# Optimization experiments

Hardware: AMD Instinct MI355X
Metric: run time of the kernel (lower is better)

The kernel has to match this reference:

```python
import jax, jax.numpy as jnp
import numpy as np

# Dims implied by init: input_dim=128, b_dim=64 -> per-branch Mamba d_model=16
D_MODEL = 16
D_STATE = 16
D_CONV = 4
D_INNER = 32   # expand * d_model
DT_RANK = 1    # ceil(d_model / 16)
EPS = 1e-5


def _ln(x, g, b):
    m = x.mean(-1, keepdims=True)
    v = x.var(-1, keepdims=True)
    return (x - m) / jnp.sqrt(v + EPS) * g + b


def _gn(x, g, b, groups):
    B, C, H, W = x.shape
    xr = x.reshape(B, groups, C // groups, H, W)
    m = xr.mean((2, 3, 4), keepdims=True)
    v = xr.var((2, 3, 4), keepdims=True)
    xr = (xr - m) / jnp.sqrt(v + EPS)
    return xr.reshape(B, C, H, W) * g[None, :, None, None] + b[None, :, None, None]


def _mamba(u, in_proj_w, conv_w, conv_b, x_proj_w, dt_proj_w, dt_proj_b, A_log, Dp, out_proj_w):
    # u: [N, L, d_model]
    N, L, _ = u.shape
    xz = u @ in_proj_w.T                       # [N, L, 2*d_inner]
    xc, zg = jnp.split(xz, 2, axis=-1)
    # causal depthwise conv1d over L
    xt = xc.transpose(0, 2, 1)                 # [N, d_inner, L]
    xt = jax.lax.conv_general_dilated(
        xt, conv_w, (1,), [(D_CONV - 1, 0)],
        dimension_numbers=('NCH', 'OIH', 'NCH'),
        feature_group_count=D_INNER)
    xt = xt + conv_b[None, :, None]
    xc = jax.nn.silu(xt).transpose(0, 2, 1)    # [N, L, d_inner]
    x_dbl = xc @ x_proj_w.T                    # [N, L, dt_rank + 2*d_state]
    dt = x_dbl[..., :DT_RANK]
    Bv = x_dbl[..., DT_RANK:DT_RANK + D_STATE]
    Cv = x_dbl[..., DT_RANK + D_STATE:]
    dt = jax.nn.softplus(dt @ dt_proj_w.T + dt_proj_b)  # [N, L, d_inner]
    A = -jnp.exp(A_log)                        # [d_inner, d_state]

    def step(h, inp):
        dt_t, B_t, C_t, x_t = inp              # [N,di],[N,ds],[N,ds],[N,di]
        dA = jnp.exp(dt_t[:, :, None] * A)     # [N, di, ds]
        h = dA * h + (dt_t * x_t)[:, :, None] * B_t[:, None, :]
        y = jnp.einsum('nds,ns->nd', h, C_t)
        return h, y

    h0 = jnp.zeros((N, D_INNER, D_STATE), u.dtype)
    xs = (dt.transpose(1, 0, 2), Bv.transpose(1, 0, 2),
          Cv.transpose(1, 0, 2), xc.transpose(1, 0, 2))
    _, ys = jax.lax.scan(step, h0, xs)         # ys: [L, N, d_inner]
    y = ys.transpose(1, 0, 2) + xc * Dp        # skip via D
    y = y * jax.nn.silu(zg)
    return y @ out_proj_w.T                    # [N, L, d_model]


def _forward(x, pre_ln_g, pre_ln_b, bott_in_w, bott_in_b,
             in_proj_w, conv_w, conv_b, x_proj_w, dt_proj_w, dt_proj_b,
             A_log, Dp, out_proj_w, post_ln_g, post_ln_b,
             bott_out_w, bott_out_b, res_scale,
             fc1_w, gn1_g, gn1_b, fc2_w, gn2_g, gn2_b):
    B, C, H, W = x.shape
    L = H * W
    # ---- PVMLayer token mixer ----
    xf = x.reshape(B, C, L).transpose(0, 2, 1)            # [B, L, C]
    z = _ln(xf, pre_ln_g, pre_ln_b)
    z = z @ bott_in_w.T + bott_in_b                       # [B, L, 64]
    # four chunks share the same Mamba weights -> batch them together
    zc = z.reshape(B, L, 4, D_MODEL).transpose(2, 0, 1, 3).reshape(4 * B, L, D_MODEL)
    m = _mamba(zc, in_proj_w, conv_w, conv_b, x_proj_w, dt_proj_w, dt_proj_b,
               A_log, Dp, out_proj_w) + zc
    z = m.reshape(4, B, L, D_MODEL).transpose(1, 2, 0, 3).reshape(B, L, 4 * D_MODEL)
    z = _ln(z, post_ln_g, post_ln_b)
    z = (z @ bott_out_w.T + bott_out_b) * res_scale       # [B, L, C]
    token = z.transpose(0, 2, 1).reshape(B, C, H, W)
    mixed = x + token                                     # PVMLayer residual (eval: drop_path=id)
    out = x + mixed                                       # PVMFormer residual
    # ---- Mlp (1x1 conv + GroupNorm) ----
    h = jnp.einsum('bchw,oc->bohw', out, fc1_w)
    h = _gn(h, gn1_g, gn1_b, 32)
    h = jax.nn.gelu(h, approximate=False)
    h = jnp.einsum('bchw,oc->bohw', h, fc2_w)
    h = _gn(h, gn2_g, gn2_b, 32)
    return out + h


def setup_inputs() -> dict:
    key = jax.random.key(0)
    ks = jax.random.split(key, 16)
    n = lambda k, s, sc=0.02: jax.random.normal(k, s, jnp.float32) * sc
    C = 128
    return {
        'x': jax.random.normal(ks[0], (8, C, 64, 64), jnp.float32),
        'pre_ln_g': jnp.ones((C,), jnp.float32),
        'pre_ln_b': jnp.zeros((C,), jnp.float32),
        'bott_in_w': n(ks[1], (64, C)),
        'bott_in_b': jnp.zeros((64,), jnp.float32),
        'in_proj_w': n(ks[2], (2 * D_INNER, D_MODEL)),
        'conv_w': n(ks[3], (D_INNER, 1, D_CONV), 0.1),
        'conv_b': jnp.zeros((D_INNER,), jnp.float32),
        'x_proj_w': n(ks[4], (DT_RANK + 2 * D_STATE, D_INNER)),
        'dt_proj_w': n(ks[5], (D_INNER, DT_RANK), 0.5),
        'dt_proj_b': n(ks[6], (D_INNER,), 0.5),
        'A_log': jnp.log(jnp.broadcast_to(jnp.arange(1.0, D_STATE + 1.0, dtype=jnp.float32), (D_INNER, D_STATE))),
        'Dp': jnp.ones((D_INNER,), jnp.float32),
        'out_proj_w': n(ks[7], (D_MODEL, D_INNER)),
        'post_ln_g': jnp.ones((64,), jnp.float32),
        'post_ln_b': jnp.zeros((64,), jnp.float32),
        'bott_out_w': n(ks[8], (C, 64)),
        'bott_out_b': jnp.zeros((C,), jnp.float32),
        'res_scale': jnp.array(0.5, jnp.float32),
        'fc1_w': n(ks[9], (4 * C, C)),
        'gn1_g': jnp.ones((4 * C,), jnp.float32),
        'gn1_b': jnp.zeros((4 * C,), jnp.float32),
        'fc2_w': n(ks[10], (C, 4 * C)),
        'gn2_g': jnp.ones((C,), jnp.float32),
        'gn2_b': jnp.zeros((C,), jnp.float32),
    }


def reference(x, pre_ln_g, pre_ln_b, bott_in_w, bott_in_b,
              in_proj_w, conv_w, conv_b, x_proj_w, dt_proj_w, dt_proj_b,
              A_log, Dp, out_proj_w, post_ln_g, post_ln_b,
              bott_out_w, bott_out_b, res_scale,
              fc1_w, gn1_g, gn1_b, fc2_w, gn2_g, gn2_b):
    return _forward(x, pre_ln_g, pre_ln_b, bott_in_w, bott_in_b,
                    in_proj_w, conv_w, conv_b, x_proj_w, dt_proj_w, dt_proj_b,
                    A_log, Dp, out_proj_w, post_ln_g, post_ln_b,
                    bott_out_w, bott_out_b, res_scale,
                    fc1_w, gn1_g, gn1_b, fc2_w, gn2_g, gn2_b)
```

## Files before the change

kernel.cpp:

```cpp
#include <hip/hip_runtime.h>
#include <hip/hip_bf16.h>
#include <math.h>

#define L4K 4096
#define NCH 32
#define CL  128
#define SPN (128*4096)

typedef __attribute__((ext_vector_type(8))) short short8;
typedef __attribute__((ext_vector_type(4))) float f32x4;

__device__ __forceinline__ unsigned short f2b(float f) {
    unsigned int u = __float_as_uint(f);
    unsigned int r = u + 0x7FFFu + ((u >> 16) & 1u);
    return (unsigned short)(r >> 16);
}
__device__ __forceinline__ float b2f(unsigned short h) {
    return __uint_as_float(((unsigned int)h) << 16);
}
__device__ __forceinline__ float rowsum16(float p) {
    int t;
    t = __builtin_amdgcn_update_dpp(0, __float_as_int(p), 0x128, 0xf, 0xf, true);
    p += __int_as_float(t);
    t = __builtin_amdgcn_update_dpp(0, __float_as_int(p), 0x124, 0xf, 0xf, true);
    p += __int_as_float(t);
    t = __builtin_amdgcn_update_dpp(0, __float_as_int(p), 0x122, 0xf, 0xf, true);
    p += __int_as_float(t);
    t = __builtin_amdgcn_update_dpp(0, __float_as_int(p), 0x121, 0xf, 0xf, true);
    p += __int_as_float(t);
    return p;
}

__global__ __launch_bounds__(256) void k1_pre(
    const float* __restrict__ x, const float* __restrict__ png, const float* __restrict__ pnb,
    const float* __restrict__ biw, const float* __restrict__ bib, const float* __restrict__ ipw,
    float* __restrict__ zc, float* __restrict__ xcp, float* __restrict__ zg)
{
    __shared__ float xs[128*32];
    __shared__ float wl[64*128];
    __shared__ float zs[32*65];
    __shared__ float ipl[64*16];
    __shared__ float pngs[128], pnbs[128];
    int tid = threadIdx.x;
    int l0 = blockIdx.x*32, b = blockIdx.y;
    const float* xb = x + (size_t)b*128*L4K;
    for (int it = 0; it < 16; ++it) {
        int f = it*256 + tid; int c = f>>5, i = f&31;
        xs[f] = xb[(size_t)c*L4K + l0 + i];
    }
    for (int f = tid; f < 8192; f += 256) wl[f] = biw[f];
    for (int f = tid; f < 1024; f += 256) ipl[f] = ipw[f];
    if (tid < 128) { pngs[tid] = png[tid]; pnbs[tid] = pnb[tid]; }
    __syncthreads();
    int i = tid & 31, q = tid >> 5;
    float s = 0.f, s2 = 0.f;
    for (int c = 0; c < 128; ++c) { float v = xs[c*32+i]; s += v; s2 = fmaf(v,v,s2); }
    float mn = s*(1.f/128.f);
    float rstd = rsqrtf(s2*(1.f/128.f) - mn*mn + 1e-5f);
    float z[8];
    #pragma unroll
    for (int jj = 0; jj < 8; ++jj) z[jj] = bib[q*8+jj];
    for (int c = 0; c < 128; ++c) {
        float xv = (xs[c*32+i] - mn)*rstd*pngs[c] + pnbs[c];
        #pragma unroll
        for (int jj = 0; jj < 8; ++jj) z[jj] = fmaf(xv, wl[(q*8+jj)*128 + c], z[jj]);
    }
    #pragma unroll
    for (int jj = 0; jj < 8; ++jj) zs[i*65 + q*8 + jj] = z[jj];
    __syncthreads();
    if (tid < 128) {
        int i2 = tid & 31, g = tid >> 5;
        int n = g*8 + b; int l = l0 + i2;
        float zv[16];
        #pragma unroll
        for (int k = 0; k < 16; ++k) zv[k] = zs[i2*65 + g*16 + k];
        float* zcb = zc + ((size_t)n*16)*L4K + l;
        #pragma unroll
        for (int k = 0; k < 16; ++k) zcb[(size_t)k*L4K] = zv[k];
        float* xo = xcp + ((size_t)n*32)*L4K + l;
        float* zo = zg  + ((size_t)n*32)*L4K + l;
        #pragma unroll
        for (int o = 0; o < 64; ++o) {
            float a = 0.f;
            #pragma unroll
            for (int k = 0; k < 16; ++k) a = fmaf(zv[k], ipl[o*16+k], a);
            if (o < 32) xo[(size_t)o*L4K] = a; else zo[(size_t)(o-32)*L4K] = a;
        }
    }
}

__global__ __launch_bounds__(128) void k2_conv(
    const float* __restrict__ xcp, const float* __restrict__ cw, const float* __restrict__ cb,
    const float* __restrict__ xpw, const float* __restrict__ dtw, const float* __restrict__ dtb,
    float* __restrict__ S)
{
    __shared__ float xt[131*33];
    __shared__ float cwl[128], cbl[32], xpl[33*32], dtwl[32], dtbl[32];
    int tid = threadIdx.x;
    int t0 = blockIdx.x*128; int n = blockIdx.y;
    const float* xb = xcp + (size_t)n*32*L4K;
    #pragma unroll 4
    for (int d = 0; d < 32; ++d) {
        int t = t0 - 3 + tid;
        xt[tid*33 + d] = (t >= 0) ? xb[(size_t)d*L4K + t] : 0.f;
        if (tid < 3) {
            int r = 128 + tid; int t2 = t0 - 3 + r;
            xt[r*33 + d] = xb[(size_t)d*L4K + t2];
        }
    }
    if (tid < 128) cwl[tid] = cw[tid];
    if (tid < 32) { cbl[tid] = cb[tid]; dtwl[tid] = dtw[tid]; dtbl[tid] = dtb[tid]; }
    for (int f = tid; f < 33*32; f += 128) xpl[f] = xpw[f];
    __syncthreads();
    int t = t0 + tid;
    float xc[32];
    #pragma unroll
    for (int d = 0; d < 32; ++d) {
        float sv = cbl[d];
        #pragma unroll
        for (int k = 0; k < 4; ++k) sv = fmaf(cwl[d*4+k], xt[(tid+k)*33 + d], sv);
        xc[d] = sv / (1.f + __expf(-sv));
    }
    float dtr = 0.f; float Bv[16], Cv[16];
    #pragma unroll
    for (int dd = 0; dd < 32; ++dd) dtr = fmaf(xc[dd], xpl[dd], dtr);
    #pragma unroll
    for (int o = 0; o < 16; ++o) {
        float a = 0.f, a2 = 0.f;
        #pragma unroll
        for (int dd = 0; dd < 32; ++dd) {
            a  = fmaf(xc[dd], xpl[(1+o)*32+dd],  a);
            a2 = fmaf(xc[dd], xpl[(17+o)*32+dd], a2);
        }
        Bv[o] = a; Cv[o] = a2;
    }
    float* Sn = S + (size_t)n*SPN + t;
    #pragma unroll
    for (int d = 0; d < 32; ++d) {
        float dv = fmaf(dtr, dtwl[d], dtbl[d]);
        float sp = fmaxf(dv, 0.f) + log1pf(__expf(-fabsf(dv)));
        Sn[(size_t)d*L4K]      = sp;
        Sn[(size_t)(32+d)*L4K] = sp * xc[d];
        Sn[(size_t)(96+d)*L4K] = xc[d];
    }
    #pragma unroll
    for (int o = 0; o < 16; ++o) {
        Sn[(size_t)(64+o)*L4K] = Bv[o];
        Sn[(size_t)(80+o)*L4K] = Cv[o];
    }
}

__global__ __launch_bounds__(512) void k3a_local(
    const float* __restrict__ S, const float* __restrict__ alog,
    float* __restrict__ chunkA, float* __restrict__ chunkH)
{
    __shared__ float2 pDT[32*130];
    __shared__ float  pB[16*132];
    int tid = threadIdx.x;
    int d = tid >> 4, s = tid & 15;
    int chunk = blockIdx.x, n = blockIdx.y;
    float A = -__expf(alog[d*16 + s]);
    const float* base = S + (size_t)n*SPN + (size_t)chunk*CL;
    {
        int sd = tid >> 4, j = tid & 15;
        const float* dtp = base + (size_t)sd*L4K + j*8;
        const float* dxp = base + (size_t)(32+sd)*L4K + j*8;
        float4 a0 = *(const float4*)(dtp);
        float4 a1 = *(const float4*)(dtp+4);
        float4 b0 = *(const float4*)(dxp);
        float4 b1 = *(const float4*)(dxp+4);
        float2* w = pDT + sd*130 + j*8;
        *(float4*)(w+0) = make_float4(a0.x,b0.x,a0.y,b0.y);
        *(float4*)(w+2) = make_float4(a0.z,b0.z,a0.w,b0.w);
        *(float4*)(w+4) = make_float4(a1.x,b1.x,a1.y,b1.y);
        *(float4*)(w+6) = make_float4(a1.z,b1.z,a1.w,b1.w);
    }
    if (tid < 256) {
        int ss = tid >> 4, j = tid & 15;
        const float* bp = base + (size_t)(64+ss)*L4K + j*8;
        float4 v0 = *(const float4*)(bp);
        float4 v1 = *(const float4*)(bp+4);
        float* w = pB + ss*132 + j*8;
        *(float4*)(w+0) = v0;
        *(float4*)(w+4) = v1;
    }
    __syncthreads();
    float h = 0.f, ap = 1.f;
    #pragma unroll 4
    for (int t = 0; t < CL; ++t) {
        float2 dd = pDT[d*130 + t];
        float Bv = pB[s*132 + t];
        float dA = __expf(dd.x * A);
        h = fmaf(dA, h, dd.y * Bv);
        ap *= dA;
    }
    size_t idx = (size_t)chunk*16384 + n*512 + tid;
    chunkA[idx] = ap;
    chunkH[idx] = h;
}

__global__ __launch_bounds__(256) void k3b_prefix(
    const float* __restrict__ chunkA, const float* __restrict__ chunkH,
    float* __restrict__ hstart)
{
    int nds = blockIdx.x*256 + threadIdx.x;
    float h = 0.f;
    hstart[nds] = 0.f;
    for (int c = 0; c < NCH-1; ++c) {
        h = fmaf(h, chunkA[(size_t)c*16384 + nds], chunkH[(size_t)c*16384 + nds]);
        hstart[(size_t)(c+1)*16384 + nds] = h;
    }
}

__global__ __launch_bounds__(512) void k3c_emit(
    const float* __restrict__ S, const float* __restrict__ alog,
    const float* __restrict__ hstart, float* __restrict__ y)
{
    __shared__ float2 pDT[32*130];
    __shared__ float2 pBC[16*130];
    int tid = threadIdx.x;
    int d = tid >> 4, s = tid & 15;
    int chunk = blockIdx.x, n = blockIdx.y;
    float A = -__expf(alog[d*16 + s]);
    const float* base = S + (size_t)n*SPN + (size_t)chunk*CL;
    float h = hstart[(size_t)chunk*16384 + n*512 + tid];
    {
        int sd = tid >> 4, j = tid & 15;
        const float* dtp = base + (size_t)sd*L4K + j*8;
        const float* dxp = base + (size_t)(32+sd)*L4K + j*8;
        float4 a0 = *(const float4*)(dtp);
        float4 a1 = *(const float4*)(dtp+4);
        float4 b0 = *(const float4*)(dxp);
        float4 b1 = *(const float4*)(dxp+4);
        float2* w = pDT + sd*130 + j*8;
        *(float4*)(w+0) = make_float4(a0.x,b0.x,a0.y,b0.y);
        *(float4*)(w+2) = make_float4(a0.z,b0.z,a0.w,b0.w);
        *(float4*)(w+4) = make_float4(a1.x,b1.x,a1.y,b1.y);
        *(float4*)(w+6) = make_float4(a1.z,b1.z,a1.w,b1.w);
    }
    if (tid < 256) {
        int ss = tid >> 4, j = tid & 15;
        const float* bp = base + (size_t)(64+ss)*L4K + j*8;
        const float* cp = base + (size_t)(80+ss)*L4K + j*8;
        float4 v0 = *(const float4*)(bp);
        float4 v1 = *(const float4*)(bp+4);
        float4 c0 = *(const float4*)(cp);
        float4 c1 = *(const float4*)(cp+4);
        float2* w = pBC + ss*130 + j*8;
        *(float4*)(w+0) = make_float4(v0.x,c0.x,v0.y,c0.y);
        *(float4*)(w+2) = make_float4(v0.z,c0.z,v0.w,c0.w);
        *(float4*)(w+4) = make_float4(v1.x,c1.x,v1.y,c1.y);
        *(float4*)(w+6) = make_float4(v1.z,c1.z,v1.w,c1.w);
    }
    __syncthreads();
    float4* yb = (float4*)(y + ((size_t)n*32 + d)*L4K + (size_t)chunk*CL);
    for (int i = 0; i < CL/4; ++i) {
        float4 yv;
        #pragma unroll
        for (int u = 0; u < 4; ++u) {
            int t = i*4 + u;
            float2 dd = pDT[d*130 + t];
            float2 bc = pBC[s*130 + t];
            float dA = __expf(dd.x * A);
            h = fmaf(dA, h, dd.y * bc.x);
            ((float*)&yv)[u] = rowsum16(h * bc.y);
        }
        if (s == 0) yb[i] = yv;
    }
}

__global__ __launch_bounds__(256) void k5_out(
    const float* __restrict__ y, const float* __restrict__ S, const float* __restrict__ zg,
    const float* __restrict__ zc, const float* __restrict__ Dp, const float* __restrict__ opw,
    float* __restrict__ m)
{
    int id = blockIdx.x*256 + threadIdx.x;
    int n = id >> 12, t = id & 4095;
    const float* yb  = y  + (size_t)n*32*L4K + t;
    const float* xcb = S  + (size_t)n*SPN + (size_t)96*L4K + t;
    const float* zgb = zg + (size_t)n*32*L4K + t;
    const float* zcb = zc + (size_t)n*16*L4K + t;
    float v[32];
    #pragma unroll
    for (int dd = 0; dd < 32; ++dd) {
        float g = zgb[(size_t)dd*L4K];
        float sig = 1.f/(1.f + __expf(-g));
        v[dd] = (yb[(size_t)dd*L4K] + xcb[(size_t)dd*L4K]*Dp[dd]) * (g*sig);
    }
    int b = n & 7, g4 = n >> 3;
    float* mp = m + ((size_t)b*64 + g4*16)*L4K + t;
    #pragma unroll
    for (int j = 0; j < 16; ++j) {
        float a = zcb[(size_t)j*L4K];
        #pragma unroll
        for (int dd = 0; dd < 32; ++dd) a = fmaf(v[dd], opw[j*32+dd], a);
        mp[(size_t)j*L4K] = a;
    }
}

__global__ __launch_bounds__(256) void k6_post(
    const float* __restrict__ m, const float* __restrict__ x,
    const float* __restrict__ pog, const float* __restrict__ pob,
    const float* __restrict__ bow, const float* __restrict__ bob,
    const float* __restrict__ rsp, float* __restrict__ outp,
    unsigned short* __restrict__ outpb)
{
    __shared__ float ms[64*65];
    __shared__ float wl[128*64];
    __shared__ float pogs[64], pobs[64];
    int tid = threadIdx.x;
    int l0 = blockIdx.x*64, b = blockIdx.y;
    for (int f = tid; f < 4096; f += 256) {
        int i = f & 63, j = f >> 6;
        ms[i*65 + j] = m[((size_t)b*64 + j)*L4K + l0 + i];
    }
    for (int f = tid; f < 8192; f += 256) wl[f] = bow[f];
    if (tid < 64) { pogs[tid] = pog[tid]; pobs[tid] = pob[tid]; }
    __syncthreads();
    float rs = rsp[0];
    int i = tid & 63, q = tid >> 6;
    float s = 0.f, s2 = 0.f;
    for (int j = 0; j < 64; ++j) { float v = ms[i*65+j]; s += v; s2 = fmaf(v,v,s2); }
    float mn = s*(1.f/64.f);
    float rstd = rsqrtf(s2*(1.f/64.f) - mn*mn + 1e-5f);
    float acc[32];
    #pragma unroll
    for (int cc = 0; cc < 32; ++cc) acc[cc] = bob[q*32+cc];
    for (int j = 0; j < 64; ++j) {
        float v = (ms[i*65+j]-mn)*rstd*pogs[j] + pobs[j];
        #pragma unroll
        for (int cc = 0; cc < 32; ++cc) acc[cc] = fmaf(v, wl[(q*32+cc)*64+j], acc[cc]);
    }
    const float* xb = x + (size_t)b*128*L4K + l0 + i;
    float* ob = outp + (size_t)b*128*L4K + l0 + i;
    unsigned short pk[32];
    #pragma unroll
    for (int cc = 0; cc < 32; ++cc) {
        int c = q*32 + cc;
        float val = 2.f*xb[(size_t)c*L4K] + acc[cc]*rs;
        ob[(size_t)c*L4K] = val;
        pk[cc] = f2b(val);
    }
    uint4* op = (uint4*)&outpb[((size_t)b*L4K + l0 + i)*128 + q*32];
    #pragma unroll
    for (int u = 0; u < 4; ++u) {
        uint4 v;
        v.x = pk[u*8+0] | ((unsigned)pk[u*8+1]<<16);
        v.y = pk[u*8+2] | ((unsigned)pk[u*8+3]<<16);
        v.z = pk[u*8+4] | ((unsigned)pk[u*8+5]<<16);
        v.w = pk[u*8+6] | ((unsigned)pk[u*8+7]<<16);
        op[u] = v;
    }
}

template<int KCHUNKS, bool OUT_BF16>
__global__ __launch_bounds__(256) void gemm_mfma(
    const unsigned short* __restrict__ Ab, const float* __restrict__ Wg,
    void* __restrict__ Dout, int Kpitch, int Npitch)
{
    __shared__ char lds[65536];
    int tid = threadIdx.x;
    int lane = tid & 63, w = tid >> 6;
    int l0 = blockIdx.x * 128, n0 = blockIdx.y * 128, b = blockIdx.z;
    size_t arow0 = (size_t)b*L4K + l0;
    int wm = (w>>1)*64, wn = (w&1)*64;
    f32x4 acc[4][4] = {};
    char* aL = lds;
    char* wL = lds + 32768;
    for (int kc = 0; kc < KCHUNKS; ++kc) {
        if (kc) __syncthreads();
        #pragma unroll
        for (int it = 0; it < 8; ++it) {
            int f = it*256 + tid;
            int row = f >> 4, kp = f & 15;
            uint4 v = *(const uint4*)&Ab[(arow0 + row)*(size_t)Kpitch + kc*128 + kp*8];
            int off = row*256 + kp*16; off ^= (row&7)<<4;
            *(uint4*)(aL + off) = v;
        }
        #pragma unroll
        for (int it = 0; it < 16; ++it) {
            int f = it*256 + tid;
            int row = f >> 5, kg = f & 31;
            float4 v = *(const float4*)&Wg[(size_t)(n0+row)*(KCHUNKS*128) + kc*128 + kg*4];
            uint2 p;
            p.x = f2b(v.x) | ((unsigned)f2b(v.y)<<16);
            p.y = f2b(v.z) | ((unsigned)f2b(v.w)<<16);
            int off = row*256 + kg*8; off ^= (row&7)<<4;
            *(uint2*)(wL + off) = p;
        }
        __syncthreads();
        #pragma unroll
        for (int ks = 0; ks < 4; ++ks) {
            short8 af[4], wf[4];
            int kb = ks*64 + (lane>>4)*16;
            #pragma unroll
            for (int mi = 0; mi < 4; ++mi) {
                int row = wm + mi*16 + (lane&15);
                int off = row*256 + kb; off ^= (row&7)<<4;
                af[mi] = *(const short8*)(aL + off);
            }
            #pragma unroll
            for (int ni = 0; ni < 4; ++ni) {
                int row = wn + ni*16 + (lane&15);
                int off = row*256 + kb; off ^= (row&7)<<4;
                wf[ni] = *(const short8*)(wL + off);
            }
            #pragma unroll
            for (int mi = 0; mi < 4; ++mi)
                #pragma unroll
                for (int ni = 0; ni < 4; ++ni)
                    acc[mi][ni] = __builtin_amdgcn_mfma_f32_16x16x32_bf16(af[mi], wf[ni], acc[mi][ni], 0, 0, 0);
        }
    }
    if (OUT_BF16) {
        __syncthreads();
        unsigned short* cL = (unsigned short*)lds;
        #pragma unroll
        for (int mi = 0; mi < 4; ++mi)
            #pragma unroll
            for (int ni = 0; ni < 4; ++ni)
                #pragma unroll
                for (int r = 0; r < 4; ++r) {
                    int row = wm + mi*16 + (lane>>4)*4 + r;
                    int col = wn + ni*16 + (lane&15);
                    cL[row*136 + col] = f2b(acc[mi][ni][r]);
                }
        __syncthreads();
        unsigned short* D = (unsigned short*)Dout;
        #pragma unroll
        for (int it = 0; it < 8; ++it) {
            int f = it*256 + tid;
            int row = f >> 4, kp = f & 15;
            uint4 v = *(const uint4*)&cL[row*136 + kp*8];
            *(uint4*)&D[(arow0 + row)*(size_t)Npitch + n0 + kp*8] = v;
        }
    } else {
        float* D = (float*)Dout;
        #pragma unroll
        for (int mi = 0; mi < 4; ++mi)
            #pragma unroll
            for (int ni = 0; ni < 4; ++ni)
                #pragma unroll
                for (int r = 0; r < 4; ++r) {
                    int row = wm + mi*16 + (lane>>4)*4 + r;
                    int col = wn + ni*16 + (lane&15);
                    D[(arow0 + row)*(size_t)Npitch + n0 + col] = acc[mi][ni][r];
                }
    }
}

__global__ __launch_bounds__(256) void k_gn1stats(
    const unsigned short* __restrict__ h, float* __restrict__ stats)
{
    __shared__ float sred[256], sred2[256];
    int tid = threadIdx.x;
    int b = blockIdx.x >> 5, g = blockIdx.x & 31;
    float s = 0.f, s2 = 0.f;
    for (int it = 0; it < 32; ++it) {
        int f = it*256 + tid;
        int l = f >> 1, half = f & 1;
        uint4 v = *(const uint4*)&h[((size_t)b*L4K + l)*512 + g*16 + half*8];
        unsigned int ws[4] = {v.x, v.y, v.z, v.w};
        #pragma unroll
        for (int u = 0; u < 4; ++u) {
            float a = b2f((unsigned short)(ws[u] & 0xFFFF));
            float c = b2f((unsigned short)(ws[u] >> 16));
            s += a + c; s2 = fmaf(a,a,s2); s2 = fmaf(c,c,s2);
        }
    }
    sred[tid] = s; sred2[tid] = s2; __syncthreads();
    for (int off = 128; off; off >>= 1) {
        if (tid < off) { sred[tid] += sred[tid+off]; sred2[tid] += sred2[tid+off]; }
        __syncthreads();
    }
    if (tid == 0) {
        float inv = 1.f/65536.f;
        float mn = sred[0]*inv;
        float var = sred2[0]*inv - mn*mn;
        stats[blockIdx.x*2]   = mn;
        stats[blockIdx.x*2+1] = rsqrtf(var + 1e-5f);
    }
}

__global__ __launch_bounds__(256) void k9_gngelu(
    unsigned short* __restrict__ h, const float* __restrict__ stats,
    const float* __restrict__ g1, const float* __restrict__ b1)
{
    size_t idx = ((size_t)blockIdx.x*256 + threadIdx.x)*8;
    int o0 = (int)(idx & 511);
    int b = (int)(idx >> 21);
    int sg = b*32 + (o0 >> 4);
    float mn = stats[sg*2], rstd = stats[sg*2+1];
    uint4 v = *(uint4*)&h[idx];
    unsigned int ws[4] = {v.x, v.y, v.z, v.w};
    unsigned int out[4];
    #pragma unroll
    for (int u = 0; u < 4; ++u) {
        float a = b2f((unsigned short)(ws[u] & 0xFFFF));
        float c = b2f((unsigned short)(ws[u] >> 16));
        int o = o0 + u*2;
        float ta = (a-mn)*rstd*g1[o]   + b1[o];
        float tc = (c-mn)*rstd*g1[o+1] + b1[o+1];
        ta = 0.5f*ta*(1.f + erff(ta*0.70710678118654752f));
        tc = 0.5f*tc*(1.f + erff(tc*0.70710678118654752f));
        out[u] = f2b(ta) | ((unsigned)f2b(tc)<<16);
    }
    uint4 r; r.x = out[0]; r.y = out[1]; r.z = out[2]; r.w = out[3];
    *(uint4*)&h[idx] = r;
}

__global__ __launch_bounds__(256) void k_gn2stats(
    const float* __restrict__ h, float* __restrict__ stats)
{
    __shared__ float sred[256], sred2[256];
    int tid = threadIdx.x;
    int b = blockIdx.x >> 5, g = blockIdx.x & 31;
    float s = 0.f, s2 = 0.f;
    for (int it = 0; it < 16; ++it) {
        int l = it*256 + tid;
        float4 v = ((const float4*)h)[((size_t)b*L4K + l)*32 + g];
        s += v.x+v.y+v.z+v.w;
        s2 = fmaf(v.x,v.x,s2); s2 = fmaf(v.y,v.y,s2); s2 = fmaf(v.z,v.z,s2); s2 = fmaf(v.w,v.w,s2);
    }
    sred[tid] = s; sred2[tid] = s2; __syncthreads();
    for (int off = 128; off; off >>= 1) {
        if (tid < off) { sred[tid] += sred[tid+off]; sred2[tid] += sred2[tid+off]; }
        __syncthreads();
    }
    if (tid == 0) {
        float inv = 1.f/16384.f;
        float mn = sred[0]*inv;
        float var = sred2[0]*inv - mn*mn;
        stats[blockIdx.x*2]   = mn;
        stats[blockIdx.x*2+1] = rsqrtf(var + 1e-5f);
    }
}

__global__ __launch_bounds__(256) void k12_final(
    const float* __restrict__ outp, const float* __restrict__ h2t,
    const float* __restrict__ stats, const float* __restrict__ g2,
    const float* __restrict__ b2, float* __restrict__ out)
{
    __shared__ float T[32*33];
    int tid = threadIdx.x;
    int l0 = blockIdx.x*32, c0 = blockIdx.y*32, b = blockIdx.z;
    {
        int i = tid >> 3, jq = tid & 7;
        float4 v = ((const float4*)h2t)[((size_t)b*L4K + l0 + i)*32 + (c0>>2) + jq];
        int sg = b*32 + (c0>>2) + jq;
        float mn = stats[sg*2], rstd = stats[sg*2+1];
        int c = c0 + jq*4;
        T[(jq*4+0)*33 + i] = (v.x-mn)*rstd*g2[c+0] + b2[c+0];
        T[(jq*4+1)*33 + i] = (v.y-mn)*rstd*g2[c+1] + b2[c+1];
        T[(jq*4+2)*33 + i] = (v.z-mn)*rstd*g2[c+2] + b2[c+2];
        T[(jq*4+3)*33 + i] = (v.w-mn)*rstd*g2[c+3] + b2[c+3];
    }
    __syncthreads();
    {
        int c = tid >> 3, iq = tid & 7;
        size_t gi = ((size_t)b*128 + c0 + c)*1024 + (l0>>2) + iq;
        float4 o = ((const float4*)outp)[gi];
        float4 r;
        r.x = o.x + T[c*33 + iq*4 + 0];
        r.y = o.y + T[c*33 + iq*4 + 1];
        r.z = o.z + T[c*33 + iq*4 + 2];
        r.w = o.w + T[c*33 + iq*4 + 3];
        ((float4*)out)[gi] = r;
    }
}

extern "C" void kernel_launch(void* const* d_in, const int* in_sizes, int n_in,
                              void* d_out, int out_size, void* d_ws, size_t ws_size,
                              hipStream_t stream) {
    (void)in_sizes; (void)n_in; (void)out_size; (void)ws_size;
    const float* x    = (const float*)d_in[0];
    const float* png  = (const float*)d_in[1];
    const float* pnb  = (const float*)d_in[2];
    const float* biw  = (const float*)d_in[3];
    const float* bib  = (const float*)d_in[4];
    const float* ipw  = (const float*)d_in[5];
    const float* cw   = (const float*)d_in[6];
    const float* cb   = (const float*)d_in[7];
    const float* xpw  = (const float*)d_in[8];
    const float* dtw  = (const float*)d_in[9];
    const float* dtb  = (const float*)d_in[10];
    const float* alog = (const float*)d_in[11];
    const float* Dp   = (const float*)d_in[12];
    const float* opw  = (const float*)d_in[13];
    const float* pog  = (const float*)d_in[14];
    const float* pob  = (const float*)d_in[15];
    const float* bow  = (const float*)d_in[16];
    const float* bob  = (const float*)d_in[17];
    const float* rsp  = (const float*)d_in[18];
    const float* f1w  = (const float*)d_in[19];
    const float* g1g  = (const float*)d_in[20];
    const float* g1b  = (const float*)d_in[21];
    const float* f2w  = (const float*)d_in[22];
    const float* g2g  = (const float*)d_in[23];
    const float* g2b  = (const float*)d_in[24];

    char* ws = (char*)d_ws;
    float* S    = (float*)(ws + 0);
    float* zc   = (float*)(ws + 67108864);
    float* zg   = (float*)(ws + 75497472);
    float* xcp  = (float*)(ws + 92274688);
    float* y    = (float*)(ws + 92274688);
    float* m    = (float*)(ws + 109051904);
    float* chA  = (float*)(ws + 109051904);
    float* chH  = (float*)(ws + 109051904 + 2097152);
    float* hst  = (float*)(ws + 109051904 + 4194304);
    float*          outp  = (float*)(ws + 0);
    unsigned short* outpb = (unsigned short*)(ws + 16777216);
    unsigned short* h1tb  = (unsigned short*)(ws + 25165824);
    float*          h2t   = (float*)(ws + 58720256);
    float*          st1   = (float*)(ws + 75497472);
    float*          st2   = (float*)(ws + 75501568);

    k1_pre<<<dim3(128,8),256,0,stream>>>(x,png,pnb,biw,bib,ipw,zc,xcp,zg);
    k2_conv<<<dim3(32,32),128,0,stream>>>(xcp,cw,cb,xpw,dtw,dtb,S);
    k3a_local<<<dim3(NCH,32),512,0,stream>>>(S,alog,chA,chH);
    k3b_prefix<<<64,256,0,stream>>>(chA,chH,hst);
    k3c_emit<<<dim3(NCH,32),512,0,stream>>>(S,alog,hst,y);
    k5_out<<<512,256,0,stream>>>(y,S,zg,zc,Dp,opw,m);
    k6_post<<<dim3(64,8),256,0,stream>>>(m,x,pog,pob,bow,bob,rsp,outp,outpb);
    gemm_mfma<1,true><<<dim3(32,4,8),256,0,stream>>>(outpb,f1w,(void*)h1tb,128,512);
    k_gn1stats<<<256,256,0,stream>>>(h1tb,st1);
    k9_gngelu<<<8192,256,0,stream>>>(h1tb,st1,g1g,g1b);
    gemm_mfma<4,false><<<dim3(32,1,8),256,0,stream>>>(h1tb,f2w,(void*)h2t,512,128);
    k_gn2stats<<<256,256,0,stream>>>(h2t,st2);
    k12_final<<<dim3(128,4,8),256,0,stream>>>(outp,h2t,st2,g2g,g2b,(float*)d_out);
}
```

Baseline: 392.9 us.

## Trim registers in conv and output kernels, halve GEMM2 tile, approximate GELU

k2_conv drops its shared-memory weight staging, reads weights straight from global memory, and computes the B and C projections in two separate loops to lower register pressure. k5_out splits each timestep's work across two threads through shared memory and launches twice the blocks. The second GEMM uses 64-row tiles so it runs twice as many blocks. The erf-based GELU is replaced with the tanh approximation built on fast exp, which changes numerics slightly.

```diff
diff --git a/kernel.cpp b/kernel.cpp
--- a/kernel.cpp
+++ b/kernel.cpp
@@ -95,7 +95,6 @@
     float* __restrict__ S)
 {
     __shared__ float xt[131*33];
-    __shared__ float cwl[128], cbl[32], xpl[33*32], dtwl[32], dtbl[32];
     int tid = threadIdx.x;
     int t0 = blockIdx.x*128; int n = blockIdx.y;
     const float* xb = xcp + (size_t)n*32*L4K;
@@ -103,50 +102,44 @@
     for (int d = 0; d < 32; ++d) {
         int t = t0 - 3 + tid;
         xt[tid*33 + d] = (t >= 0) ? xb[(size_t)d*L4K + t] : 0.f;
-        if (tid < 3) {
-            int r = 128 + tid; int t2 = t0 - 3 + r;
-            xt[r*33 + d] = xb[(size_t)d*L4K + t2];
-        }
-    }
-    if (tid < 128) cwl[tid] = cw[tid];
-    if (tid < 32) { cbl[tid] = cb[tid]; dtwl[tid] = dtw[tid]; dtbl[tid] = dtb[tid]; }
-    for (int f = tid; f < 33*32; f += 128) xpl[f] = xpw[f];
-    __syncthreads();
-    int t = t0 + tid;
+        if (tid < 3) xt[(128+tid)*33 + d] = xb[(size_t)d*L4K + t0 + 125 + tid];
+    }
+    __syncthreads();
     float xc[32];
     #pragma unroll
     for (int d = 0; d < 32; ++d) {
-        float sv = cbl[d];
-        #pragma unroll
-        for (int k = 0; k < 4; ++k) sv = fmaf(cwl[d*4+k], xt[(tid+k)*33 + d], sv);
-        xc[d] = sv / (1.f + __expf(-sv));
-    }
-    float dtr = 0.f; float Bv[16], Cv[16];
-    #pragma unroll
-    for (int dd = 0; dd < 32; ++dd) dtr = fmaf(xc[dd], xpl[dd], dtr);
-    #pragma unroll
-    for (int o = 0; o < 16; ++o) {
-        float a = 0.f, a2 = 0.f;
-        #pragma unroll
-        for (int dd = 0; dd < 32; ++dd) {
-            a  = fmaf(xc[dd], xpl[(1+o)*32+dd],  a);
-            a2 = fmaf(xc[dd], xpl[(17+o)*32+dd], a2);
-        }
-        Bv[o] = a; Cv[o] = a2;
-    }
-    float* Sn = S + (size_t)n*SPN + t;
+        float sv = cb[d];
+        #pragma unroll
+        for (int k = 0; k < 4; ++k) sv = fmaf(cw[d*4+k], xt[(tid+k)*33 + d], sv);
+        float e = __expf(-sv);
+        xc[d] = __fdividef(sv, 1.f + e);
+    }
+    float* Sn = S + (size_t)n*SPN + t0 + tid;
+    float dtr = 0.f;
+    #pragma unroll
+    for (int dd = 0; dd < 32; ++dd) dtr = fmaf(xc[dd], xpw[dd], dtr);
     #pragma unroll
     for (int d = 0; d < 32; ++d) {
-        float dv = fmaf(dtr, dtwl[d], dtbl[d]);
-        float sp = fmaxf(dv, 0.f) + log1pf(__expf(-fabsf(dv)));
+        float dv = fmaf(dtr, dtw[d], dtb[d]);
+        float e = __expf(-fabsf(dv));
+        float sp = fmaxf(dv, 0.f) + __logf(1.f + e);
         Sn[(size_t)d*L4K]      = sp;
         Sn[(size_t)(32+d)*L4K] = sp * xc[d];
         Sn[(size_t)(96+d)*L4K] = xc[d];
     }
     #pragma unroll
     for (int o = 0; o < 16; ++o) {
-        Sn[(size_t)(64+o)*L4K] = Bv[o];
-        Sn[(size_t)(80+o)*L4K] = Cv[o];
+        float a = 0.f;
+        #pragma unroll
+        for (int dd = 0; dd < 32; ++dd) a = fmaf(xc[dd], xpw[(1+o)*32+dd], a);
+        Sn[(size_t)(64+o)*L4K] = a;
+    }
+    #pragma unroll
+    for (int o = 0; o < 16; ++o) {
+        float a = 0.f;
+        #pragma unroll
+        for (int dd = 0; dd < 32; ++dd) a = fmaf(xc[dd], xpw[(17+o)*32+dd], a);
+        Sn[(size_t)(80+o)*L4K] = a;
     }
 }
 
@@ -274,26 +267,31 @@
     const float* __restrict__ zc, const float* __restrict__ Dp, const float* __restrict__ opw,
     float* __restrict__ m)
 {
-    int id = blockIdx.x*256 + threadIdx.x;
+    __shared__ float vs[128*33];
+    int tid = threadIdx.x;
+    int tl = tid & 127, p = tid >> 7;
+    int id = blockIdx.x*128 + tl;
     int n = id >> 12, t = id & 4095;
     const float* yb  = y  + (size_t)n*32*L4K + t;
     const float* xcb = S  + (size_t)n*SPN + (size_t)96*L4K + t;
     const float* zgb = zg + (size_t)n*32*L4K + t;
     const float* zcb = zc + (size_t)n*16*L4K + t;
-    float v[32];
-    #pragma unroll
-    for (int dd = 0; dd < 32; ++dd) {
+    #pragma unroll
+    for (int dd2 = 0; dd2 < 16; ++dd2) {
+        int dd = p*16 + dd2;
         float g = zgb[(size_t)dd*L4K];
         float sig = 1.f/(1.f + __expf(-g));
-        v[dd] = (yb[(size_t)dd*L4K] + xcb[(size_t)dd*L4K]*Dp[dd]) * (g*sig);
-    }
+        vs[tl*33 + dd] = (yb[(size_t)dd*L4K] + xcb[(size_t)dd*L4K]*Dp[dd]) * (g*sig);
+    }
+    __syncthreads();
     int b = n & 7, g4 = n >> 3;
     float* mp = m + ((size_t)b*64 + g4*16)*L4K + t;
     #pragma unroll
-    for (int j = 0; j < 16; ++j) {
+    for (int jj = 0; jj < 8; ++jj) {
+        int j = p*8 + jj;
         float a = zcb[(size_t)j*L4K];
         #pragma unroll
-        for (int dd = 0; dd < 32; ++dd) a = fmaf(v[dd], opw[j*32+dd], a);
+        for (int dd = 0; dd < 32; ++dd) a = fmaf(vs[tl*33+dd], opw[j*32+dd], a);
         mp[(size_t)j*L4K] = a;
     }
 }
@@ -353,24 +351,25 @@
     }
 }
 
-template<int KCHUNKS, bool OUT_BF16>
+template<int KCHUNKS, int BM, bool OUT_BF16>
 __global__ __launch_bounds__(256) void gemm_mfma(
     const unsigned short* __restrict__ Ab, const float* __restrict__ Wg,
     void* __restrict__ Dout, int Kpitch, int Npitch)
 {
-    __shared__ char lds[65536];
+    __shared__ char lds[BM*256 + 32768];
+    constexpr int MI = BM/32;
     int tid = threadIdx.x;
     int lane = tid & 63, w = tid >> 6;
-    int l0 = blockIdx.x * 128, n0 = blockIdx.y * 128, b = blockIdx.z;
+    int l0 = blockIdx.x * BM, n0 = blockIdx.y * 128, b = blockIdx.z;
     size_t arow0 = (size_t)b*L4K + l0;
-    int wm = (w>>1)*64, wn = (w&1)*64;
-    f32x4 acc[4][4] = {};
+    int wm = (w>>1)*(BM/2), wn = (w&1)*64;
+    f32x4 acc[MI][4] = {};
     char* aL = lds;
-    char* wL = lds + 32768;
+    char* wL = lds + BM*256;
     for (int kc = 0; kc < KCHUNKS; ++kc) {
         if (kc) __syncthreads();
         #pragma unroll
-        for (int it = 0; it < 8; ++it) {
+        for (int it = 0; it < BM/16; ++it) {
             int f = it*256 + tid;
             int row = f >> 4, kp = f & 15;
             uint4 v = *(const uint4*)&Ab[(arow0 + row)*(size_t)Kpitch + kc*128 + kp*8];
@@ -391,10 +390,10 @@
         __syncthreads();
         #pragma unroll
         for (int ks = 0; ks < 4; ++ks) {
-            short8 af[4], wf[4];
+            short8 af[MI], wf[4];
             int kb = ks*64 + (lane>>4)*16;
             #pragma unroll
-            for (int mi = 0; mi < 4; ++mi) {
+            for (int mi = 0; mi < MI; ++mi) {
                 int row = wm + mi*16 + (lane&15);
                 int off = row*256 + kb; off ^= (row&7)<<4;
                 af[mi] = *(const short8*)(aL + off);
@@ -406,7 +405,7 @@
                 wf[ni] = *(const short8*)(wL + off);
             }
             #pragma unroll
-            for (int mi = 0; mi < 4; ++mi)
+            for (int mi = 0; mi < MI; ++mi)
                 #pragma unroll
                 for (int ni = 0; ni < 4; ++ni)
                     acc[mi][ni] = __builtin_amdgcn_mfma_f32_16x16x32_bf16(af[mi], wf[ni], acc[mi][ni], 0, 0, 0);
@@ -416,7 +415,7 @@
         __syncthreads();
         unsigned short* cL = (unsigned short*)lds;
         #pragma unroll
-        for (int mi = 0; mi < 4; ++mi)
+        for (int mi = 0; mi < MI; ++mi)
             #pragma unroll
             for (int ni = 0; ni < 4; ++ni)
                 #pragma unroll
@@ -428,7 +427,7 @@
         __syncthreads();
         unsigned short* D = (unsigned short*)Dout;
         #pragma unroll
-        for (int it = 0; it < 8; ++it) {
+        for (int it = 0; it < BM/16; ++it) {
             int f = it*256 + tid;
             int row = f >> 4, kp = f & 15;
             uint4 v = *(const uint4*)&cL[row*136 + kp*8];
@@ -437,7 +436,7 @@
     } else {
         float* D = (float*)Dout;
         #pragma unroll
-        for (int mi = 0; mi < 4; ++mi)
+        for (int mi = 0; mi < MI; ++mi)
             #pragma unroll
             for (int ni = 0; ni < 4; ++ni)
                 #pragma unroll
@@ -501,8 +500,11 @@
         int o = o0 + u*2;
         float ta = (a-mn)*rstd*g1[o]   + b1[o];
         float tc = (c-mn)*rstd*g1[o+1] + b1[o+1];
-        ta = 0.5f*ta*(1.f + erff(ta*0.70710678118654752f));
-        tc = 0.5f*tc*(1.f + erff(tc*0.70710678118654752f));
+        float za = 0.7978845608f*fmaf(0.044715f*ta, ta*ta, ta);
+        float zc2 = 0.7978845608f*fmaf(0.044715f*tc, tc*tc, tc);
+        float ea = __expf(-2.f*za), ec = __expf(-2.f*zc2);
+        ta = ta * __fdividef(1.f, 1.f + ea);
+        tc = tc * __fdividef(1.f, 1.f + ec);
         out[u] = f2b(ta) | ((unsigned)f2b(tc)<<16);
     }
     uint4 r; r.x = out[0]; r.y = out[1]; r.z = out[2]; r.w = out[3];
@@ -621,12 +623,12 @@
     k3a_local<<<dim3(NCH,32),512,0,stream>>>(S,alog,chA,chH);
     k3b_prefix<<<64,256,0,stream>>>(chA,chH,hst);
     k3c_emit<<<dim3(NCH,32),512,0,stream>>>(S,alog,hst,y);
-    k5_out<<<512,256,0,stream>>>(y,S,zg,zc,Dp,opw,m);
+    k5_out<<<1024,256,0,stream>>>(y,S,zg,zc,Dp,opw,m);
     k6_post<<<dim3(64,8),256,0,stream>>>(m,x,pog,pob,bow,bob,rsp,outp,outpb);
-    gemm_mfma<1,true><<<dim3(32,4,8),256,0,stream>>>(outpb,f1w,(void*)h1tb,128,512);
+    gemm_mfma<1,128,true><<<dim3(32,4,8),256,0,stream>>>(outpb,f1w,(void*)h1tb,128,512);
     k_gn1stats<<<256,256,0,stream>>>(h1tb,st1);
     k9_gngelu<<<8192,256,0,stream>>>(h1tb,st1,g1g,g1b);
-    gemm_mfma<4,false><<<dim3(32,1,8),256,0,stream>>>(h1tb,f2w,(void*)h2t,512,128);
+    gemm_mfma<4,64,false><<<dim3(64,1,8),256,0,stream>>>(h1tb,f2w,(void*)h2t,512,128);
     k_gn2stats<<<256,256,0,stream>>>(h2t,st2);
     k12_final<<<dim3(128,4,8),256,0,stream>>>(outp,h2t,st2,g2g,g2b,(float*)d_out);
 }
```

After: 381.3 us. 3.0% less time.
